# Kernel tuning notes

Hardware: AMD Instinct MI355X
Metric: run time of the kernel (lower is better)

Reference implementation:

```python
import jax, jax.numpy as jnp
import numpy as np

B, T, C = 8, 512, 2048          # batch streams, qlen, hidden_size
H, Z = 32, 64                   # num_heads, head_size; A = H*Z = attention_hidden_size
A = H * Z
TMX, TDX = 32, 64               # TIME_MIX_EXTRA_DIM, TIME_DECAY_EXTRA_DIM
EPS = 1e-5 * 8.0**2             # ln_x eps = 1e-5 * head_size_divisor**2


def setup_inputs() -> dict:
    key = jax.random.key(0)
    ks = jax.random.split(key, 24)
    def rn(i, shape, scale=1.0):
        return jax.random.normal(ks[i], shape, jnp.float32) * scale
    inv_c = 1.0 / np.sqrt(C)
    return {
        "hidden_states": rn(0, (B * T, C)),
        "positions": jnp.zeros((B * T,), jnp.int32),
        "input_kv_state": jnp.zeros((B, H, Z, Z), jnp.float32),
        "input_shift_state": rn(1, (B, C)),
        "time_maa_x": rn(2, (1, 1, C), 0.1),
        "time_maa_w": rn(3, (1, 1, C), 0.1),
        "time_maa_k": rn(4, (1, 1, C), 0.1),
        "time_maa_v": rn(5, (1, 1, C), 0.1),
        "time_maa_r": rn(6, (1, 1, C), 0.1),
        "time_maa_g": rn(7, (1, 1, C), 0.1),
        "time_maa_w1": rn(8, (C, TMX * 5), inv_c),
        "time_maa_w2": rn(9, (5, TMX, C), 1.0 / np.sqrt(TMX)),
        "time_decay": rn(10, (1, 1, A), 0.5),
        "time_decay_w1": rn(11, (C, TDX), inv_c),
        "time_decay_w2": rn(12, (TDX, A), 0.01),
        "time_faaaa": rn(13, (H, Z), 0.1),
        "W_r": rn(14, (C, A), inv_c),
        "W_k": rn(15, (C, A), inv_c),
        "W_v": rn(16, (C, A), inv_c),
        "W_g": rn(17, (C, A), inv_c),
        "W_o": rn(18, (A, C), inv_c),
        "ln_w": 1.0 + rn(19, (C,), 0.1),
        "ln_b": rn(20, (C,), 0.1),
    }


def _rwkv6_forward(hidden_states, positions, input_kv_state, input_shift_state,
                   time_maa_x, time_maa_w, time_maa_k, time_maa_v, time_maa_r,
                   time_maa_g, time_maa_w1, time_maa_w2, time_decay,
                   time_decay_w1, time_decay_w2, time_faaaa,
                   W_r, W_k, W_v, W_g, W_o, ln_w, ln_b):
    x = hidden_states.reshape(B, T, C)
    pos0_is_zero = positions.reshape(B, T)[:, 0] == 0
    reset = jnp.where(pos0_is_zero, -100.0, 0.0)  # [B]
    # kill shift state for fresh sequences (matches * exp(-100))
    shift = input_shift_state * jnp.exp(reset)[:, None]  # [B, C]

    # token-shift mixing (shift state broadcast over T, as in source)
    xx = shift[:, None, :] - x  # [B, T, C]
    xxx = x + xx * time_maa_x
    mix = jnp.tanh(xxx @ time_maa_w1).reshape(B, T, 5, TMX)
    mix = jnp.einsum('btfe,fec->fbtc', mix, time_maa_w2)  # [5, B, T, C]
    mw, mk, mv, mr, mg = mix

    td_in = x + xx * (time_maa_w + mw)
    kx = x + xx * (time_maa_k + mk)
    vx = x + xx * (time_maa_v + mv)
    rx = x + xx * (time_maa_r + mr)
    gx = x + xx * (time_maa_g + mg)

    r = rx @ W_r
    k = kx @ W_k
    v = vx @ W_v
    g = jax.nn.silu(gx @ W_g)  # [B, T, A]

    w = time_decay + jnp.tanh(td_in @ time_decay_w1) @ time_decay_w2
    w = -jnp.exp(w.astype(jnp.float32))  # log-decay, [B, T, A]

    # split heads -> [T, B, H, Z] for scan
    def to_tbhz(a):
        return a.reshape(B, T, H, Z).transpose(1, 0, 2, 3)
    r_s, k_s, v_s, w_s = to_tbhz(r), to_tbhz(k), to_tbhz(v), to_tbhz(w)
    # zero out carried state at t=0 for fresh sequences
    w_s = w_s.at[0].add(reset[:, None, None])

    u = time_faaaa  # [H, Z]

    def step(S, rkvw):
        # S: [B, H, K, V] (key-dim x value-dim state)
        r_t, k_t, v_t, w_t = rkvw  # each [B, H, Z]
        kv = k_t[..., :, None] * v_t[..., None, :]  # [B, H, K, V]
        o = jnp.einsum('bhk,bhkv->bhv', r_t, S + u[None, :, :, None] * kv)
        S = jnp.exp(w_t)[..., None] * S + kv
        return S, o

    S_out, o = jax.lax.scan(step, input_kv_state, (r_s, k_s, v_s, w_s))
    xo = o.transpose(1, 0, 2, 3).reshape(B * T, C)  # [B*T, C]

    # GroupNorm over heads (num_groups = H)
    xg = xo.reshape(B * T, H, Z)
    mu = xg.mean(-1, keepdims=True)
    var = xg.var(-1, keepdims=True)
    xn = ((xg - mu) * jax.lax.rsqrt(var + EPS)).reshape(B * T, C) * ln_w + ln_b

    out = (xn.reshape(B, T, C) * g) @ W_o  # [B, T, C]
    return out.reshape(B * T, C)


def reference(hidden_states, positions, input_kv_state, input_shift_state,
              time_maa_x, time_maa_w, time_maa_k, time_maa_v, time_maa_r,
              time_maa_g, time_maa_w1, time_maa_w2, time_decay,
              time_decay_w1, time_decay_w2, time_faaaa,
              W_r, W_k, W_v, W_g, W_o, ln_w, ln_b):
    return _rwkv6_forward(hidden_states, positions, input_kv_state,
                          input_shift_state, time_maa_x, time_maa_w,
                          time_maa_k, time_maa_v, time_maa_r, time_maa_g,
                          time_maa_w1, time_maa_w2, time_decay, time_decay_w1,
                          time_decay_w2, time_faaaa, W_r, W_k, W_v, W_g, W_o,
                          ln_w, ln_b)
```

## Files before the change

### kernel.cpp

```cpp
#include <hip/hip_runtime.h>
#include <cmath>

#define NB 8
#define NT 512
#define NC 2048
#define NH 32
#define NZ 64
static constexpr float GN_EPS = 1e-5f * 64.0f;

typedef _Float16 f16;
typedef __attribute__((ext_vector_type(8))) _Float16 f16x8;
typedef __attribute__((ext_vector_type(4))) _Float16 f16x4;
typedef __attribute__((ext_vector_type(4))) float f4;

__global__ void k_transpose_cast(const float* __restrict__ in, f16* __restrict__ out,
                                 int R, int Cc) {
  __shared__ float tile[32][33];
  int c0 = blockIdx.x * 32, r0 = blockIdx.y * 32;
  int tx = threadIdx.x, ty = threadIdx.y;
#pragma unroll
  for (int i = 0; i < 4; ++i)
    tile[ty + i * 8][tx] = in[(size_t)(r0 + ty + i * 8) * Cc + c0 + tx];
  __syncthreads();
#pragma unroll
  for (int i = 0; i < 4; ++i)
    out[(size_t)(c0 + ty + i * 8) * R + r0 + tx] = (f16)tile[tx][ty + i * 8];
}

__global__ void k_transpose_split(const float* __restrict__ in, f16* __restrict__ ohi,
                                  f16* __restrict__ olo, int R, int Cc) {
  __shared__ float tile[32][33];
  int c0 = blockIdx.x * 32, r0 = blockIdx.y * 32;
  int tx = threadIdx.x, ty = threadIdx.y;
#pragma unroll
  for (int i = 0; i < 4; ++i)
    tile[ty + i * 8][tx] = in[(size_t)(r0 + ty + i * 8) * Cc + c0 + tx];
  __syncthreads();
#pragma unroll
  for (int i = 0; i < 4; ++i) {
    float v = tile[tx][ty + i * 8];
    f16 h = (f16)v;
    size_t o = (size_t)(c0 + ty + i * 8) * R + r0 + tx;
    ohi[o] = h;
    olo[o] = (f16)(v - (float)h);
  }
}

__global__ void k_xxx(const float* __restrict__ hs, const float* __restrict__ shift_st,
                      const int* __restrict__ positions, const float* __restrict__ maa_x,
                      float* __restrict__ xxx) {
  int i = blockIdx.x * blockDim.x + threadIdx.x;
  int idx = i * 4;
  int c = idx & (NC - 1);
  int t = idx >> 11;
  int b = t >> 9;
  float er = (positions[b * NT] == 0) ? expf(-100.0f) : 1.0f;
  const float4 x = *(const float4*)(hs + idx);
  const float4 sh = *(const float4*)(shift_st + b * NC + c);
  const float4 mx = *(const float4*)(maa_x + c);
  float4 o;
  o.x = x.x + (sh.x * er - x.x) * mx.x;
  o.y = x.y + (sh.y * er - x.y) * mx.y;
  o.z = x.z + (sh.z * er - x.z) * mx.z;
  o.w = x.w + (sh.w * er - x.w) * mx.w;
  *(float4*)(xxx + idx) = o;
}

static __device__ __forceinline__ void split4(const float4 v, int base, f16x8& hi, f16x8& lo) {
  float x[4] = {v.x, v.y, v.z, v.w};
#pragma unroll
  for (int j = 0; j < 4; ++j) {
    f16 h = (f16)x[j];
    hi[base + j] = h;
    lo[base + j] = (f16)(x[j] - (float)h);
  }
}

__global__ __launch_bounds__(64) void k_mix1_split(const float* __restrict__ A,
                                                   const f16* __restrict__ Bhi,
                                                   const f16* __restrict__ Blo,
                                                   float* __restrict__ out) {
  int m0 = blockIdx.x * 16, n0 = blockIdx.y * 16;
  int lane = threadIdx.x, lr = lane & 15, kq = lane >> 4;
  f4 acc = {0.f, 0.f, 0.f, 0.f};
  const float* ap = A + (size_t)(m0 + lr) * 2048 + kq * 8;
  const f16* bh0 = Bhi + (size_t)(n0 + lr) * 2048 + kq * 8;
  const f16* bl0 = Blo + (size_t)(n0 + lr) * 2048 + kq * 8;
  for (int k0 = 0; k0 < 2048; k0 += 32) {
    f16x8 ah, al;
    split4(*(const float4*)(ap + k0), 0, ah, al);
    split4(*(const float4*)(ap + k0 + 4), 4, ah, al);
    f16x8 bh = *(const f16x8*)(bh0 + k0);
    f16x8 bl = *(const f16x8*)(bl0 + k0);
    acc = __builtin_amdgcn_mfma_f32_16x16x32_f16(ah, bh, acc, 0, 0, 0);
    acc = __builtin_amdgcn_mfma_f32_16x16x32_f16(ah, bl, acc, 0, 0, 0);
    acc = __builtin_amdgcn_mfma_f32_16x16x32_f16(al, bh, acc, 0, 0, 0);
  }
#pragma unroll
  for (int r = 0; r < 4; ++r)
    out[(size_t)(m0 + kq * 4 + r) * 160 + n0 + lr] = tanhf(acc[r]);
}

__global__ __launch_bounds__(64) void k_tmp5_split(const float* __restrict__ mixb,
    const f16* __restrict__ Bhi, const f16* __restrict__ Blo,
    const float* __restrict__ hs, const float* __restrict__ shift_st,
    const int* __restrict__ positions,
    const float* __restrict__ maa_w, const float* __restrict__ maa_k,
    const float* __restrict__ maa_v, const float* __restrict__ maa_r,
    const float* __restrict__ maa_g,
    float* __restrict__ tdin, f16* __restrict__ kx, f16* __restrict__ vx,
    f16* __restrict__ rx, f16* __restrict__ gx) {
  int m0 = blockIdx.x * 16, n0 = blockIdx.y * 16;
  int lane = threadIdx.x, lr = lane & 15, kq = lane >> 4;
  f4 acc[5];
#pragma unroll
  for (int f = 0; f < 5; ++f) acc[f] = (f4){0.f, 0.f, 0.f, 0.f};
  const float* ap = mixb + (size_t)(m0 + lr) * 160 + kq * 8;
#pragma unroll
  for (int f = 0; f < 5; ++f) {
    f16x8 ah, al;
    split4(*(const float4*)(ap + f * 32), 0, ah, al);
    split4(*(const float4*)(ap + f * 32 + 4), 4, ah, al);
    size_t bi = ((size_t)f * 2048 + n0 + lr) * 32 + kq * 8;
    f16x8 bh = *(const f16x8*)(Bhi + bi);
    f16x8 bl = *(const f16x8*)(Blo + bi);
    acc[f] = __builtin_amdgcn_mfma_f32_16x16x32_f16(ah, bh, acc[f], 0, 0, 0);
    acc[f] = __builtin_amdgcn_mfma_f32_16x16x32_f16(ah, bl, acc[f], 0, 0, 0);
    acc[f] = __builtin_amdgcn_mfma_f32_16x16x32_f16(al, bh, acc[f], 0, 0, 0);
  }
  int c = n0 + lr;
  float mw = maa_w[c], mk = maa_k[c], mv = maa_v[c], mr = maa_r[c], mg = maa_g[c];
#pragma unroll
  for (int r = 0; r < 4; ++r) {
    int t = m0 + kq * 4 + r;
    int b = t >> 9;
    float er = (positions[b * NT] == 0) ? expf(-100.0f) : 1.0f;
    float x = hs[(size_t)t * NC + c];
    float xxv = shift_st[b * NC + c] * er - x;
    size_t oi = (size_t)t * NC + c;
    tdin[oi] = x + xxv * (mw + acc[0][r]);
    kx[oi] = (f16)(x + xxv * (mk + acc[1][r]));
    vx[oi] = (f16)(x + xxv * (mv + acc[2][r]));
    rx[oi] = (f16)(x + xxv * (mr + acc[3][r]));
    gx[oi] = (f16)(x + xxv * (mg + acc[4][r]));
  }
}

__global__ __launch_bounds__(64) void k_wd1_split(const float* __restrict__ A,
                                                  const f16* __restrict__ Bhi,
                                                  const f16* __restrict__ Blo,
                                                  float* __restrict__ out) {
  int m0 = blockIdx.x * 16, n0 = blockIdx.y * 16;
  int lane = threadIdx.x, lr = lane & 15, kq = lane >> 4;
  f4 acc = {0.f, 0.f, 0.f, 0.f};
  const float* ap = A + (size_t)(m0 + lr) * 2048 + kq * 8;
  const f16* bh0 = Bhi + (size_t)(n0 + lr) * 2048 + kq * 8;
  const f16* bl0 = Blo + (size_t)(n0 + lr) * 2048 + kq * 8;
  for (int k0 = 0; k0 < 2048; k0 += 32) {
    f16x8 ah, al;
    split4(*(const float4*)(ap + k0), 0, ah, al);
    split4(*(const float4*)(ap + k0 + 4), 4, ah, al);
    f16x8 bh = *(const f16x8*)(bh0 + k0);
    f16x8 bl = *(const f16x8*)(bl0 + k0);
    acc = __builtin_amdgcn_mfma_f32_16x16x32_f16(ah, bh, acc, 0, 0, 0);
    acc = __builtin_amdgcn_mfma_f32_16x16x32_f16(ah, bl, acc, 0, 0, 0);
    acc = __builtin_amdgcn_mfma_f32_16x16x32_f16(al, bh, acc, 0, 0, 0);
  }
#pragma unroll
  for (int r = 0; r < 4; ++r)
    out[(size_t)(m0 + kq * 4 + r) * 64 + n0 + lr] = tanhf(acc[r]);
}

__global__ __launch_bounds__(64) void k_wdecay_split(const float* __restrict__ A,
                                                     const f16* __restrict__ Bhi,
                                                     const f16* __restrict__ Blo,
                                                     const float* __restrict__ time_decay,
                                                     float* __restrict__ wout) {
  int m0 = blockIdx.x * 16, n0 = blockIdx.y * 16;
  int lane = threadIdx.x, lr = lane & 15, kq = lane >> 4;
  f4 acc = {0.f, 0.f, 0.f, 0.f};
#pragma unroll
  for (int kk = 0; kk < 2; ++kk) {
    f16x8 ah, al;
    const float* ap = A + (size_t)(m0 + lr) * 64 + kk * 32 + kq * 8;
    split4(*(const float4*)ap, 0, ah, al);
    split4(*(const float4*)(ap + 4), 4, ah, al);
    size_t bi = (size_t)(n0 + lr) * 64 + kk * 32 + kq * 8;
    f16x8 bh = *(const f16x8*)(Bhi + bi);
    f16x8 bl = *(const f16x8*)(Blo + bi);
    acc = __builtin_amdgcn_mfma_f32_16x16x32_f16(ah, bh, acc, 0, 0, 0);
    acc = __builtin_amdgcn_mfma_f32_16x16x32_f16(ah, bl, acc, 0, 0, 0);
    acc = __builtin_amdgcn_mfma_f32_16x16x32_f16(al, bh, acc, 0, 0, 0);
  }
  int c = n0 + lr;
  float td = time_decay[c];
#pragma unroll
  for (int r = 0; r < 4; ++r) {
    int t = m0 + kq * 4 + r;
    wout[(size_t)t * NC + c] = -expf(td + acc[r]);
  }
}

#define GBM 128
#define GBN 128
#define GBK 64
#define LDK 72

template <int EPI>
__global__ __launch_bounds__(256) void k_gemm_big(const f16* __restrict__ A,
                                                  const f16* __restrict__ Bt,
                                                  float* __restrict__ Cf,
                                                  f16* __restrict__ Cb, int K) {
  __shared__ __align__(16) f16 As[GBM][LDK];
  __shared__ __align__(16) f16 Bs[GBN][LDK];
  int n0 = blockIdx.x * GBN, m0 = blockIdx.y * GBM;
  int tid = threadIdx.x;
  int wid = tid >> 6, lane = tid & 63;
  int wr = wid >> 1, wc = wid & 1;
  int lr = lane & 15, kq = lane >> 4;
  int srow = tid >> 3, sseg = tid & 7;
  f4 acc[4][4];
#pragma unroll
  for (int m = 0; m < 4; ++m)
#pragma unroll
    for (int n = 0; n < 4; ++n) acc[m][n] = (f4){0.f, 0.f, 0.f, 0.f};

  const f16* aptr = A + (size_t)(m0 + srow) * K + sseg * 8;
  const f16* bptr = Bt + (size_t)(n0 + srow) * K + sseg * 8;

  f16x8 ra[4], rb[4];
#pragma unroll
  for (int i = 0; i < 4; ++i) {
    ra[i] = *(const f16x8*)(aptr + (size_t)i * 32 * K);
    rb[i] = *(const f16x8*)(bptr + (size_t)i * 32 * K);
  }
  int niter = K / GBK;
  for (int it = 0; it < niter; ++it) {
    __syncthreads();
#pragma unroll
    for (int i = 0; i < 4; ++i) {
      *(f16x8*)&As[srow + i * 32][sseg * 8] = ra[i];
      *(f16x8*)&Bs[srow + i * 32][sseg * 8] = rb[i];
    }
    __syncthreads();
    if (it + 1 < niter) {
      int k0 = (it + 1) * GBK;
#pragma unroll
      for (int i = 0; i < 4; ++i) {
        ra[i] = *(const f16x8*)(aptr + k0 + (size_t)i * 32 * K);
        rb[i] = *(const f16x8*)(bptr + k0 + (size_t)i * 32 * K);
      }
    }
#pragma unroll
    for (int kk = 0; kk < 2; ++kk) {
      f16x8 af[4], bfv[4];
#pragma unroll
      for (int m = 0; m < 4; ++m)
        af[m] = *(const f16x8*)&As[wr * 64 + m * 16 + lr][kk * 32 + kq * 8];
#pragma unroll
      for (int n = 0; n < 4; ++n)
        bfv[n] = *(const f16x8*)&Bs[wc * 64 + n * 16 + lr][kk * 32 + kq * 8];
#pragma unroll
      for (int m = 0; m < 4; ++m)
#pragma unroll
        for (int n = 0; n < 4; ++n)
          acc[m][n] = __builtin_amdgcn_mfma_f32_16x16x32_f16(af[m], bfv[n], acc[m][n], 0, 0, 0);
    }
  }
#pragma unroll
  for (int m = 0; m < 4; ++m) {
    int row0 = m0 + wr * 64 + m * 16 + kq * 4;
#pragma unroll
    for (int n = 0; n < 4; ++n) {
      int col = n0 + wc * 64 + n * 16 + lr;
#pragma unroll
      for (int r = 0; r < 4; ++r) {
        float v = acc[m][n][r];
        size_t oi = (size_t)(row0 + r) * NC + col;
        if (EPI == 0) {
          Cf[oi] = v;
        } else {
          float s = v / (1.0f + expf(-v));
          Cb[oi] = (f16)s;
        }
      }
    }
  }
}

__global__ __launch_bounds__(256) void k_scanA(
    const float* rb, const float* __restrict__ kb,
    const float* __restrict__ vb, const float* __restrict__ wb,
    const float* __restrict__ kvstate, const int* __restrict__ positions,
    const float* __restrict__ faaaa, f16* __restrict__ o,
    float* rtil, float* __restrict__ Ebuf, float* __restrict__ Dbuf) {
  int blk = blockIdx.x;
  int bh = blk >> 3, c = blk & 7;
  int b = bh >> 5, h = bh & 31;
  int tid = threadIdx.x;
  int grp = tid >> 6, zz = tid & 63;
  __shared__ __align__(16) float rkew[64][4];
  __shared__ float vL[64];
  __shared__ float opart[4][64];
  float S[16], u[16];
  float Pw = 1.0f;
  if (c == 0) {
    const float* S0 = kvstate + (size_t)bh * 4096;
#pragma unroll
    for (int j = 0; j < 16; ++j) S[j] = S0[(grp * 16 + j) * 64 + zz];
  } else {
#pragma unroll
    for (int j = 0; j < 16; ++j) S[j] = 0.f;
  }
#pragma unroll
  for (int j = 0; j < 16; ++j) u[j] = faaaa[h * NZ + grp * 16 + j];
  float reset = (positions[b * NT] == 0) ? -100.0f : 0.0f;
  const size_t base = ((size_t)(b * NT) + c * 64) * NC + h * NZ + zz;
  float val;
  {
    if (grp == 0) val = rb[base];
    else if (grp == 1) val = kb[base];
    else if (grp == 2) val = wb[base];
    else val = vb[base];
  }
  for (int t = 0; t < 64; ++t) {
    float myval = val;
    if (grp == 2) {
      if (c == 0 && t == 0) myval += reset;
      myval = expf(myval);
    }
    if (grp == 3) vL[zz] = myval;
    else rkew[zz][grp] = myval;
    __syncthreads();
    if (t + 1 < 64) {
      size_t idx = base + (size_t)(t + 1) * NC;
      if (grp == 0) val = rb[idx];
      else if (grp == 1) val = kb[idx];
      else if (grp == 2) val = wb[idx];
      else val = vb[idx];
    }
    {
      int kw = grp * 16 + (zz & 15);
      float rw = rkew[kw][0];
      float ew = rkew[kw][2];
      if (c > 0 && zz < 16)
        rtil[base - zz + (size_t)t * NC + kw] = rw * Pw;
      Pw *= ew;
    }
    float vv = vL[zz];
    float op = 0.f;
#pragma unroll
    for (int j = 0; j < 16; ++j) {
      f4 q = *(const f4*)&rkew[grp * 16 + j][0];
      float kv = q[1] * vv;
      op = fmaf(q[0], fmaf(u[j], kv, S[j]), op);
      S[j] = fmaf(q[2], S[j], kv);
    }
    opart[grp][zz] = op;
    __syncthreads();
    if (grp == 0) {
      float oo = opart[0][zz] + opart[1][zz] + opart[2][zz] + opart[3][zz];
      o[base + (size_t)t * NC] = (f16)oo;
    }
  }
  if (c < 7) {
    float* E = Ebuf + ((size_t)bh * 7 + c) * 4096;
#pragma unroll
    for (int j = 0; j < 16; ++j) E[(grp * 16 + j) * 64 + zz] = S[j];
  }
  if (zz < 16) Dbuf[((size_t)bh * 8 + c) * 64 + grp * 16 + zz] = Pw;
}

__global__ __launch_bounds__(256) void k_comb(float* __restrict__ Ebuf,
                                              const float* __restrict__ Dbuf) {
  int bh = blockIdx.x, tid = threadIdx.x;
  int k = tid >> 2, v0 = (tid & 3) * 16;
  float* base = Ebuf + (size_t)bh * 7 * 4096;
  float S[16];
#pragma unroll
  for (int j = 0; j < 16; ++j) S[j] = base[k * 64 + v0 + j];
  for (int c = 2; c <= 7; ++c) {
    float d = Dbuf[((size_t)bh * 8 + (c - 1)) * 64 + k];
    float* slot = base + (size_t)(c - 1) * 4096;
#pragma unroll
    for (int j = 0; j < 16; ++j) {
      S[j] = fmaf(d, S[j], slot[k * 64 + v0 + j]);
      slot[k * 64 + v0 + j] = S[j];
    }
  }
}

__global__ __launch_bounds__(256) void k_fix(const float* __restrict__ rtil,
                                             const float* __restrict__ Ebuf,
                                             f16* __restrict__ o) {
  int blk = blockIdx.x;
  int bh = blk / 7, cm = blk - bh * 7;
  int c = cm + 1;
  int b = bh >> 5, h = bh & 31;
  __shared__ float Rs[64][65];
  __shared__ float Ss[64][65];
  int tid = threadIdx.x;
  const float* rsrc = rtil + ((size_t)(b * NT) + c * 64) * NC + h * NZ;
  const float* ssrc = Ebuf + ((size_t)bh * 7 + cm) * 4096;
#pragma unroll
  for (int q = 0; q < 4; ++q) {
    int li = tid * 4 + q;
    int rr = li >> 4, cc = (li & 15) * 4;
    float4 x = *(const float4*)(rsrc + (size_t)rr * NC + cc);
    Rs[rr][cc] = x.x; Rs[rr][cc + 1] = x.y; Rs[rr][cc + 2] = x.z; Rs[rr][cc + 3] = x.w;
    float4 y = *(const float4*)(ssrc + rr * 64 + cc);
    Ss[rr][cc] = y.x; Ss[rr][cc + 1] = y.y; Ss[rr][cc + 2] = y.z; Ss[rr][cc + 3] = y.w;
  }
  __syncthreads();
  int t = tid >> 2, v0 = (tid & 3) * 16;
  float acc[16];
#pragma unroll
  for (int j = 0; j < 16; ++j) acc[j] = 0.f;
  for (int k = 0; k < 64; ++k) {
    float rv = Rs[t][k];
#pragma unroll
    for (int j = 0; j < 16; ++j) acc[j] = fmaf(rv, Ss[k][v0 + j], acc[j]);
  }
  f16* op = o + ((size_t)(b * NT) + c * 64 + t) * NC + h * NZ + v0;
  f16x8 o0 = *(f16x8*)op, o1 = *(f16x8*)(op + 8);
#pragma unroll
  for (int j = 0; j < 8; ++j) {
    o0[j] = (f16)((float)o0[j] + acc[j]);
    o1[j] = (f16)((float)o1[j] + acc[j + 8]);
  }
  *(f16x8*)op = o0;
  *(f16x8*)(op + 8) = o1;
}

__global__ __launch_bounds__(256) void k_gnorm(const f16* __restrict__ xo, const f16* __restrict__ g,
    const float* __restrict__ ln_w, const float* __restrict__ ln_b, f16* __restrict__ y) {
  int t = blockIdx.x;
  int tid = threadIdx.x;
  int c = tid * 8;
  f16x8 xv8 = *(const f16x8*)(xo + (size_t)t * NC + c);
  float xv[8];
#pragma unroll
  for (int j = 0; j < 8; ++j) xv[j] = (float)xv8[j];
  float s = 0.f, ss = 0.f;
#pragma unroll
  for (int j = 0; j < 8; ++j) { s += xv[j]; ss += xv[j] * xv[j]; }
  s += __shfl_xor(s, 1); ss += __shfl_xor(ss, 1);
  s += __shfl_xor(s, 2); ss += __shfl_xor(ss, 2);
  s += __shfl_xor(s, 4); ss += __shfl_xor(ss, 4);
  float mu = s * (1.0f / 64.0f);
  float var = ss * (1.0f / 64.0f) - mu * mu;
  float rstd = rsqrtf(var + GN_EPS);
  f16x8 gv = *(const f16x8*)(g + (size_t)t * NC + c);
  f16x8 ov;
#pragma unroll
  for (int j = 0; j < 8; ++j) {
    float xn = (xv[j] - mu) * rstd * ln_w[c + j] + ln_b[c + j];
    ov[j] = (f16)(xn * (float)gv[j]);
  }
  *(f16x8*)(y + (size_t)t * NC + c) = ov;
}

extern "C" void kernel_launch(void* const* d_in, const int* in_sizes, int n_in,
                              void* d_out, int out_size, void* d_ws, size_t ws_size,
                              hipStream_t stream) {
  const float* hs = (const float*)d_in[0];
  const int* positions = (const int*)d_in[1];
  const float* kvstate = (const float*)d_in[2];
  const float* shift_st = (const float*)d_in[3];
  const float* maa_x = (const float*)d_in[4];
  const float* maa_w = (const float*)d_in[5];
  const float* maa_k = (const float*)d_in[6];
  const float* maa_v = (const float*)d_in[7];
  const float* maa_r = (const float*)d_in[8];
  const float* maa_g = (const float*)d_in[9];
  const float* maa_w1 = (const float*)d_in[10];
  const float* maa_w2 = (const float*)d_in[11];
  const float* time_decay = (const float*)d_in[12];
  const float* decay_w1 = (const float*)d_in[13];
  const float* decay_w2 = (const float*)d_in[14];
  const float* faaaa = (const float*)d_in[15];
  const float* W_r = (const float*)d_in[16];
  const float* W_k = (const float*)d_in[17];
  const float* W_v = (const float*)d_in[18];
  const float* W_g = (const float*)d_in[19];
  const float* W_o = (const float*)d_in[20];
  const float* ln_w = (const float*)d_in[21];
  const float* ln_b = (const float*)d_in[22];

  char* ws = (char*)d_ws;
  size_t off = 0;
  auto alloc = [&](size_t n) {
    char* p = ws + off;
    off += (n + 255) & ~(size_t)255;
    return p;
  };
  f16* w1t_hi = (f16*)alloc(160ull * 2048 * 2);
  f16* w1t_lo = (f16*)alloc(160ull * 2048 * 2);
  f16* w2t_hi = (f16*)alloc(5ull * 2048 * 32 * 2);
  f16* w2t_lo = (f16*)alloc(5ull * 2048 * 32 * 2);
  f16* dw1t_hi = (f16*)alloc(64ull * 2048 * 2);
  f16* dw1t_lo = (f16*)alloc(64ull * 2048 * 2);
  f16* dw2t_hi = (f16*)alloc(2048ull * 64 * 2);
  f16* dw2t_lo = (f16*)alloc(2048ull * 64 * 2);
  float* mixb = (float*)alloc(4096ull * 160 * 4);
  float* wd1 = (float*)alloc(4096ull * 64 * 4);
  char* R_A = alloc(4096ull * 2048 * 4);
  char* R_B = alloc(4096ull * 2048 * 4);
  char* R_C = alloc(4096ull * 2048 * 4);
  char* R_D = alloc(4096ull * 2048 * 4);
  char* R_E = alloc(4096ull * 2048 * 2);
  char* F12 = alloc(4096ull * 2048 * 4);
  char* F3 = alloc(4096ull * 2048 * 2);
  char* F4 = alloc(4096ull * 2048 * 2);

  float* xxx = (float*)R_A;
  float* tdin = (float*)R_A;
  float* wbuf = (float*)R_A;
  float* rbuf = (float*)R_B;
  float* kbuf = (float*)R_C;
  float* vbuf = (float*)R_D;
  f16* wstage = (f16*)R_E;
  f16* obuf = (f16*)R_E;
  f16* kx = (f16*)F12;
  f16* vx = (f16*)(F12 + 4096ull * 2048 * 2);
  float* Ebuf = (float*)F12;
  float* Dbuf = (float*)(F12 + 29360128);
  f16* rx = (f16*)F3;
  f16* gbuf = (f16*)F3;
  f16* gx = (f16*)F4;
  f16* wt_o = (f16*)F4;

  dim3 tb(32, 8);
  k_transpose_split<<<dim3(5, 64), tb, 0, stream>>>(maa_w1, w1t_hi, w1t_lo, 2048, 160);
  for (int f = 0; f < 5; ++f)
    k_transpose_split<<<dim3(64, 1), tb, 0, stream>>>(maa_w2 + (size_t)f * 32 * 2048,
        w2t_hi + (size_t)f * 2048 * 32, w2t_lo + (size_t)f * 2048 * 32, 32, 2048);
  k_transpose_split<<<dim3(2, 64), tb, 0, stream>>>(decay_w1, dw1t_hi, dw1t_lo, 2048, 64);
  k_transpose_split<<<dim3(64, 2), tb, 0, stream>>>(decay_w2, dw2t_hi, dw2t_lo, 64, 2048);

  k_xxx<<<8192, 256, 0, stream>>>(hs, shift_st, positions, maa_x, xxx);
  k_mix1_split<<<dim3(256, 10), 64, 0, stream>>>(xxx, w1t_hi, w1t_lo, mixb);
  k_tmp5_split<<<dim3(256, 128), 64, 0, stream>>>(mixb, w2t_hi, w2t_lo, hs, shift_st,
      positions, maa_w, maa_k, maa_v, maa_r, maa_g, tdin, kx, vx, rx, gx);
  k_wd1_split<<<dim3(256, 4), 64, 0, stream>>>(tdin, dw1t_hi, dw1t_lo, wd1);
  k_wdecay_split<<<dim3(256, 128), 64, 0, stream>>>(wd1, dw2t_hi, dw2t_lo, time_decay, wbuf);

  dim3 gg(2048 / GBN, 4096 / GBM);
  k_transpose_cast<<<dim3(64, 64), tb, 0, stream>>>(W_r, wstage, 2048, 2048);
  k_gemm_big<0><<<gg, 256, 0, stream>>>(rx, wstage, rbuf, nullptr, 2048);
  k_transpose_cast<<<dim3(64, 64), tb, 0, stream>>>(W_k, wstage, 2048, 2048);
  k_gemm_big<0><<<gg, 256, 0, stream>>>(kx, wstage, kbuf, nullptr, 2048);
  k_transpose_cast<<<dim3(64, 64), tb, 0, stream>>>(W_v, wstage, 2048, 2048);
  k_gemm_big<0><<<gg, 256, 0, stream>>>(vx, wstage, vbuf, nullptr, 2048);
  k_transpose_cast<<<dim3(64, 64), tb, 0, stream>>>(W_g, wstage, 2048, 2048);
  k_gemm_big<2><<<gg, 256, 0, stream>>>(gx, wstage, nullptr, gbuf, 2048);
  k_transpose_cast<<<dim3(64, 64), tb, 0, stream>>>(W_o, wt_o, 2048, 2048);

  k_scanA<<<2048, 256, 0, stream>>>(rbuf, kbuf, vbuf, wbuf, kvstate, positions, faaaa,
                                    obuf, rbuf, Ebuf, Dbuf);
  k_comb<<<256, 256, 0, stream>>>(Ebuf, Dbuf);
  k_fix<<<1792, 256, 0, stream>>>(rbuf, Ebuf, obuf);

  k_gnorm<<<4096, 256, 0, stream>>>(obuf, gbuf, ln_w, ln_b, obuf);
  k_gemm_big<0><<<gg, 256, 0, stream>>>(obuf, wt_o, (float*)d_out, nullptr, 2048);
}
```

Before: 712.9 us.

## Load GEMM tiles directly to LDS and rewrite the chunked scan as single-wave

The big GEMM now stages A and B tiles with global_load_lds (direct global-to-LDS) instead of register prefetch plus explicit LDS stores, and it drops the row padding. The chunked WKV scan becomes a 64-thread kernel in which each thread holds a full column of the state in registers. The bonus (u) term is computed with a wave-shuffle reduction, which removes the cross-group partial-output reduction and its shared-memory traffic. The risks are losing the overlap between the next tile's loads and the current MFMA work, LDS bank conflicts from the unpadded rows, and higher register pressure and lower parallelism in the scan.

```diff
diff --git a/kernel.cpp b/kernel.cpp
--- a/kernel.cpp
+++ b/kernel.cpp
@@ -12,6 +12,12 @@
 typedef __attribute__((ext_vector_type(8))) _Float16 f16x8;
 typedef __attribute__((ext_vector_type(4))) _Float16 f16x4;
 typedef __attribute__((ext_vector_type(4))) float f4;
+
+static __device__ __forceinline__ void gload16(const void* gp, void* lp) {
+  __builtin_amdgcn_global_load_lds(
+      (const __attribute__((address_space(1))) void*)gp,
+      (__attribute__((address_space(3))) void*)lp, 16, 0, 0);
+}
 
 __global__ void k_transpose_cast(const float* __restrict__ in, f16* __restrict__ out,
                                  int R, int Cc) {
@@ -204,53 +210,37 @@
 #define GBM 128
 #define GBN 128
 #define GBK 64
-#define LDK 72
 
 template <int EPI>
 __global__ __launch_bounds__(256) void k_gemm_big(const f16* __restrict__ A,
                                                   const f16* __restrict__ Bt,
                                                   float* __restrict__ Cf,
                                                   f16* __restrict__ Cb, int K) {
-  __shared__ __align__(16) f16 As[GBM][LDK];
-  __shared__ __align__(16) f16 Bs[GBN][LDK];
+  __shared__ __align__(16) f16 As[GBM][GBK];
+  __shared__ __align__(16) f16 Bs[GBN][GBK];
   int n0 = blockIdx.x * GBN, m0 = blockIdx.y * GBM;
   int tid = threadIdx.x;
   int wid = tid >> 6, lane = tid & 63;
   int wr = wid >> 1, wc = wid & 1;
   int lr = lane & 15, kq = lane >> 4;
-  int srow = tid >> 3, sseg = tid & 7;
+  const f16* aL = A + (size_t)(m0 + wid * 32 + (lane >> 3)) * K + (lane & 7) * 8;
+  const f16* bL = Bt + (size_t)(n0 + wid * 32 + (lane >> 3)) * K + (lane & 7) * 8;
   f4 acc[4][4];
 #pragma unroll
   for (int m = 0; m < 4; ++m)
 #pragma unroll
     for (int n = 0; n < 4; ++n) acc[m][n] = (f4){0.f, 0.f, 0.f, 0.f};
 
-  const f16* aptr = A + (size_t)(m0 + srow) * K + sseg * 8;
-  const f16* bptr = Bt + (size_t)(n0 + srow) * K + sseg * 8;
-
-  f16x8 ra[4], rb[4];
-#pragma unroll
-  for (int i = 0; i < 4; ++i) {
-    ra[i] = *(const f16x8*)(aptr + (size_t)i * 32 * K);
-    rb[i] = *(const f16x8*)(bptr + (size_t)i * 32 * K);
-  }
   int niter = K / GBK;
   for (int it = 0; it < niter; ++it) {
+    int k0 = it * GBK;
     __syncthreads();
 #pragma unroll
     for (int i = 0; i < 4; ++i) {
-      *(f16x8*)&As[srow + i * 32][sseg * 8] = ra[i];
-      *(f16x8*)&Bs[srow + i * 32][sseg * 8] = rb[i];
+      gload16(aL + k0 + (size_t)i * 8 * K, &As[wid * 32 + i * 8][0]);
+      gload16(bL + k0 + (size_t)i * 8 * K, &Bs[wid * 32 + i * 8][0]);
     }
     __syncthreads();
-    if (it + 1 < niter) {
-      int k0 = (it + 1) * GBK;
-#pragma unroll
-      for (int i = 0; i < 4; ++i) {
-        ra[i] = *(const f16x8*)(aptr + k0 + (size_t)i * 32 * K);
-        rb[i] = *(const f16x8*)(bptr + k0 + (size_t)i * 32 * K);
-      }
-    }
 #pragma unroll
     for (int kk = 0; kk < 2; ++kk) {
       f16x8 af[4], bfv[4];
@@ -288,7 +278,7 @@
   }
 }
 
-__global__ __launch_bounds__(256) void k_scanA(
+__global__ __launch_bounds__(64) void k_scanB(
     const float* rb, const float* __restrict__ kb,
     const float* __restrict__ vb, const float* __restrict__ wb,
     const float* __restrict__ kvstate, const int* __restrict__ positions,
@@ -297,78 +287,62 @@
   int blk = blockIdx.x;
   int bh = blk >> 3, c = blk & 7;
   int b = bh >> 5, h = bh & 31;
-  int tid = threadIdx.x;
-  int grp = tid >> 6, zz = tid & 63;
-  __shared__ __align__(16) float rkew[64][4];
-  __shared__ float vL[64];
-  __shared__ float opart[4][64];
-  float S[16], u[16];
-  float Pw = 1.0f;
+  int zz = threadIdx.x;
+  __shared__ __align__(16) float shR[64];
+  __shared__ __align__(16) float shE[64];
+  __shared__ __align__(16) float shK[64];
+  float S[64];
   if (c == 0) {
     const float* S0 = kvstate + (size_t)bh * 4096;
 #pragma unroll
-    for (int j = 0; j < 16; ++j) S[j] = S0[(grp * 16 + j) * 64 + zz];
+    for (int j = 0; j < 64; ++j) S[j] = S0[j * 64 + zz];
   } else {
 #pragma unroll
-    for (int j = 0; j < 16; ++j) S[j] = 0.f;
-  }
-#pragma unroll
-  for (int j = 0; j < 16; ++j) u[j] = faaaa[h * NZ + grp * 16 + j];
+    for (int j = 0; j < 64; ++j) S[j] = 0.f;
+  }
+  float u = faaaa[h * 64 + zz];
   float reset = (positions[b * NT] == 0) ? -100.0f : 0.0f;
-  const size_t base = ((size_t)(b * NT) + c * 64) * NC + h * NZ + zz;
-  float val;
-  {
-    if (grp == 0) val = rb[base];
-    else if (grp == 1) val = kb[base];
-    else if (grp == 2) val = wb[base];
-    else val = vb[base];
-  }
+  const size_t base = ((size_t)(b * NT) + c * 64) * NC + h * 64 + zz;
+  float vr = rb[base], vk = kb[base], vw = wb[base], vv = vb[base];
+  float Pw = 1.0f;
   for (int t = 0; t < 64; ++t) {
-    float myval = val;
-    if (grp == 2) {
-      if (c == 0 && t == 0) myval += reset;
-      myval = expf(myval);
-    }
-    if (grp == 3) vL[zz] = myval;
-    else rkew[zz][grp] = myval;
-    __syncthreads();
+    float nr = 0.f, nk = 0.f, nw = 0.f, nv = 0.f;
     if (t + 1 < 64) {
       size_t idx = base + (size_t)(t + 1) * NC;
-      if (grp == 0) val = rb[idx];
-      else if (grp == 1) val = kb[idx];
-      else if (grp == 2) val = wb[idx];
-      else val = vb[idx];
+      nr = rb[idx]; nk = kb[idx]; nw = wb[idx]; nv = vb[idx];
     }
-    {
-      int kw = grp * 16 + (zz & 15);
-      float rw = rkew[kw][0];
-      float ew = rkew[kw][2];
-      if (c > 0 && zz < 16)
-        rtil[base - zz + (size_t)t * NC + kw] = rw * Pw;
-      Pw *= ew;
+    float ww = vw;
+    if (c == 0 && t == 0) ww += reset;
+    float ew = expf(ww);
+    shR[zz] = vr; shE[zz] = ew; shK[zz] = vk;
+    float q = vr * u * vk;
+    q += __shfl_xor(q, 1);  q += __shfl_xor(q, 2);  q += __shfl_xor(q, 4);
+    q += __shfl_xor(q, 8);  q += __shfl_xor(q, 16); q += __shfl_xor(q, 32);
+    __syncthreads();
+    if (c > 0) rtil[base + (size_t)t * NC] = vr * Pw;
+    Pw *= ew;
+    float oacc = vv * q;
+#pragma unroll
+    for (int k0 = 0; k0 < 64; k0 += 4) {
+      f4 r4 = *(const f4*)&shR[k0];
+      f4 e4 = *(const f4*)&shE[k0];
+      f4 k4 = *(const f4*)&shK[k0];
+#pragma unroll
+      for (int j = 0; j < 4; ++j) {
+        oacc = fmaf(r4[j], S[k0 + j], oacc);
+        S[k0 + j] = fmaf(e4[j], S[k0 + j], k4[j] * vv);
+      }
     }
-    float vv = vL[zz];
-    float op = 0.f;
-#pragma unroll
-    for (int j = 0; j < 16; ++j) {
-      f4 q = *(const f4*)&rkew[grp * 16 + j][0];
-      float kv = q[1] * vv;
-      op = fmaf(q[0], fmaf(u[j], kv, S[j]), op);
-      S[j] = fmaf(q[2], S[j], kv);
-    }
-    opart[grp][zz] = op;
+    o[base + (size_t)t * NC] = (f16)oacc;
     __syncthreads();
-    if (grp == 0) {
-      float oo = opart[0][zz] + opart[1][zz] + opart[2][zz] + opart[3][zz];
-      o[base + (size_t)t * NC] = (f16)oo;
-    }
+    vr = nr; vk = nk; vw = nw; vv = nv;
   }
   if (c < 7) {
     float* E = Ebuf + ((size_t)bh * 7 + c) * 4096;
 #pragma unroll
-    for (int j = 0; j < 16; ++j) E[(grp * 16 + j) * 64 + zz] = S[j];
-  }
-  if (zz < 16) Dbuf[((size_t)bh * 8 + c) * 64 + grp * 16 + zz] = Pw;
+    for (int j = 0; j < 64; ++j) E[j * 64 + zz] = S[j];
+  }
+  Dbuf[((size_t)bh * 8 + c) * 64 + zz] = Pw;
 }
 
 __global__ __launch_bounds__(256) void k_comb(float* __restrict__ Ebuf,
@@ -556,8 +530,8 @@
   k_gemm_big<2><<<gg, 256, 0, stream>>>(gx, wstage, nullptr, gbuf, 2048);
   k_transpose_cast<<<dim3(64, 64), tb, 0, stream>>>(W_o, wt_o, 2048, 2048);
 
-  k_scanA<<<2048, 256, 0, stream>>>(rbuf, kbuf, vbuf, wbuf, kvstate, positions, faaaa,
-                                    obuf, rbuf, Ebuf, Dbuf);
+  k_scanB<<<2048, 64, 0, stream>>>(rbuf, kbuf, vbuf, wbuf, kvstate, positions, faaaa,
+                                   obuf, rbuf, Ebuf, Dbuf);
   k_comb<<<256, 256, 0, stream>>>(Ebuf, Dbuf);
   k_fix<<<1792, 256, 0, stream>>>(rbuf, Ebuf, obuf);
 
```

New measurement: 693.1 us. 2.8% less time.
